# Optimization experiments

Hardware: AMD Instinct MI355X
Metric: run time of the kernel (lower is better)

Reference implementation:

```python
import jax, jax.numpy as jnp
import numpy as np
import math

B = 1048576
BG_RES = 512
NUM_LEVELS = 2
POWER = 4
MIPNOISE = 0.5
INIT_VAL = -2.0


def cube_face_uv(v):
    # v: [N,3] direction vectors. OpenGL cubemap face convention
    # (faces: 0:+x 1:-x 2:+y 3:-y 4:+z 5:-z), as used by nvdiffrast 'cube'.
    x, y, z = v[:, 0], v[:, 1], v[:, 2]
    ax, ay, az = jnp.abs(x), jnp.abs(y), jnp.abs(z)
    is_x = (ax >= ay) & (ax >= az)
    is_y = (~is_x) & (ay >= az)
    face = jnp.where(is_x, jnp.where(x >= 0, 0, 1),
                     jnp.where(is_y, jnp.where(y >= 0, 2, 3),
                               jnp.where(z >= 0, 4, 5))).astype(jnp.int32)
    ma = jnp.where(is_x, ax, jnp.where(is_y, ay, az))
    sc = jnp.where(is_x, jnp.where(x >= 0, -z, z),
                   jnp.where(is_y, x, jnp.where(z >= 0, x, -x)))
    tc = jnp.where(is_x, -y, jnp.where(is_y, jnp.where(y >= 0, z, -z), -y))
    u = 0.5 * (sc / ma + 1.0)
    t = 0.5 * (tc / ma + 1.0)
    return face, u, t


def build_pyramid(tex):
    # tex: [6,R,R,3] -> list of 2x2 box-filtered mips down to 1x1 (nvdiffrast style)
    levels = [tex]
    t = tex
    while t.shape[1] > 1:
        R = t.shape[1]
        t = t.reshape(6, R // 2, 2, R // 2, 2, 3).mean(axis=(2, 4))
        levels.append(t)
    return levels


def bilinear(tex, face, u, v):
    # tex: [6,R,R,3]; face/u/v: [N]. Clamp-to-edge bilinear per selected face.
    R = tex.shape[1]
    x = u * R - 0.5
    y = v * R - 0.5
    x0f = jnp.floor(x); y0f = jnp.floor(y)
    fx = (x - x0f)[:, None]; fy = (y - y0f)[:, None]
    x0 = jnp.clip(x0f.astype(jnp.int32), 0, R - 1)
    y0 = jnp.clip(y0f.astype(jnp.int32), 0, R - 1)
    x1 = jnp.clip(x0f.astype(jnp.int32) + 1, 0, R - 1)
    y1 = jnp.clip(y0f.astype(jnp.int32) + 1, 0, R - 1)
    flat = tex.reshape(6 * R * R, 3)
    base = face * (R * R)
    g00 = flat[base + y0 * R + x0]
    g01 = flat[base + y0 * R + x1]
    g10 = flat[base + y1 * R + x0]
    g11 = flat[base + y1 * R + x1]
    return ((1 - fx) * (1 - fy) * g00 + fx * (1 - fy) * g01 +
            (1 - fx) * fy * g10 + fx * fy * g11)


def sample_cubemap(tex6, face, u, v, mip):
    # trilinear: bilinear in two adjacent mips, lerp by fractional mip level
    levels = build_pyramid(tex6)
    lmax = float(len(levels) - 1)
    m = jnp.clip(mip, 0.0, lmax)
    out = jnp.zeros((face.shape[0], 3), tex6.dtype)
    for l, t in enumerate(levels):
        wl = jnp.clip(1.0 - jnp.abs(m - l), 0.0, 1.0)  # (1-f)/f trilinear weights
        out = out + wl[:, None] * bilinear(t, face, u, v)
    return out


def setup_inputs() -> dict:
    key = jax.random.key(0)
    k1, k2, k3, k4, k5 = jax.random.split(key, 5)
    viewdirs = jax.random.normal(k1, (B, 3), dtype=jnp.float32)
    viewdirs = viewdirs / jnp.linalg.norm(viewdirs, axis=-1, keepdims=True)
    saSample = jax.random.normal(k2, (B,), dtype=jnp.float32)
    noise_u = jax.random.uniform(k3, (B,), dtype=jnp.float32)
    # parameters (init_val*ones/(num_levels-i) in torch; perturbed for nontrivial grads)
    bg_mat0 = (INIT_VAL * jnp.ones((1, 6, 128, 128, 3), jnp.float32)
               + 0.1 * jax.random.normal(k4, (1, 6, 128, 128, 3), jnp.float32))
    bg_mat1 = (INIT_VAL / 2.0 * jnp.ones((1, 6, 512, 512, 3), jnp.float32)
               + 0.1 * jax.random.normal(k5, (1, 6, 512, 512, 3), jnp.float32))
    return {
        "viewdirs": viewdirs,
        "saSample": saSample,
        "noise_u": noise_u,
        "bg_mat0": bg_mat0,
        "bg_mat1": bg_mat1,
        "brightness": jnp.asarray(0.0, jnp.float32),
        "mul": jnp.asarray(1.0, jnp.float32),
        "mipbias": jnp.asarray(0.5, jnp.float32),
    }


def reference(viewdirs, saSample, noise_u, bg_mat0, bg_mat1, brightness, mul, mipbias):
    h = w = BG_RES  # from bg_mats[-1]
    # sa2mip
    distortion = 1.0 / jnp.max(jnp.abs(viewdirs), axis=-1)  # 1/||u||_inf
    saTexel = distortion / h / w
    miplevel = ((saSample - jnp.log(saTexel)) / math.log(POWER) / 2.0
                + mipbias + MIPNOISE * noise_u)
    miplevel = jnp.maximum(miplevel, 0.0)

    face, u, t = cube_face_uv(viewdirs)
    sumemb = sample_cubemap(bg_mat0[0], face, u, t, miplevel)  # mip 1 (128)
    sumemb = sumemb + sample_cubemap(bg_mat1[0], face, u, t, miplevel)  # mip 0 (512)

    # activation == 'identity' branch: exp(x).clip(0.01, 1000)
    img = jnp.clip(jnp.exp(jnp.clip(brightness, -1.0, 2.0) + mul * sumemb), 0.01, 1000.0)
    return img
```

## Files before the change

kernel.cpp:

```cpp
#include <hip/hip_runtime.h>
#include <math.h>


#define NPYR1_4 524286
#define FPB 557052
#define NFP 36780
#define NSTANDALONE 35988

__device__ __constant__ int OFFS0[7] = {0, 24576, 30720, 32256, 32640, 32736, 32760};
__device__ __constant__ int OFFS1[9] = {0, 393216, 491520, 516096, 522240,
                                        523776, 524160, 524256, 524280};
static const int H_OFFS0[5] = {0, 24576, 30720, 32256, 32640};
static const int H_OFFS1[5] = {0, 393216, 491520, 516096, 522240};

__device__ __constant__ int FPO1C[7] = {0, 25350, 31884, 33618, 34104, 34254, 34308};
__device__ __constant__ int FPO0C[5] = {34332, 36066, 36552, 36702, 36756};

__device__ __constant__ int FPB1T[4] = {33618, 34104, 34254, 34308};
__device__ __constant__ int FPB0T[2] = {36702, 36756};

__device__ __constant__ int S_START[7] = {0, 25350, 31884, 33618, 35352, 35838, 35988};
__device__ __constant__ int S_R[6]     = {64, 32, 16, 16, 8, 4};
__device__ __constant__ int S_SRC[6]   = {491520, 516096, 522240, 555006, 556542, 556926};
__device__ __constant__ int S_DST[6]   = {0, 25350, 31884, 34332, 36066, 36552};

struct PyrArgs {
    const float* src;
    float4* dst[5];
    int R;
    int tpf;
};

__global__ __launch_bounds__(256) void pyr_kernel(PyrArgs a0, PyrArgs a1, int split) {
    __shared__ float raw[32 * 96];
    __shared__ float4 A[16 * 16];
    __shared__ float4 Bb[8 * 8];

    PyrArgs a = (blockIdx.x < (unsigned)split) ? a0 : a1;
    int bid = (blockIdx.x < (unsigned)split) ? blockIdx.x : blockIdx.x - split;

    const int tpf = a.tpf, R = a.R;
    const int face = bid / (tpf * tpf);
    const int tif = bid - face * tpf * tpf;
    const int ty = tif / tpf, tx = tif - (tif / tpf) * tpf;
    const int tid = threadIdx.x;
    const int baseY = ty * 32, baseX = tx * 32;

    const float4* src4 = (const float4*)a.src;
    float4* raw4 = (float4*)raw;
    for (int idx = tid; idx < 768; idx += 256) {
        int r = idx / 24, c = idx - (idx / 24) * 24;
        size_t fidx = ((size_t)(face * R + baseY + r) * R + baseX) * 3;
        raw4[r * 24 + c] = src4[fidx / 4 + c];
    }
    __syncthreads();

    {
        int Rg = R >> 1;
        float4* dst = a.dst[0];
        int ly = tid >> 4, lx = tid & 15;
        const float* r0 = raw + (2 * ly) * 96 + 6 * lx;
        const float* r1 = r0 + 96;
        float4 s = make_float4(0.25f * (r0[0] + r0[3] + r1[0] + r1[3]),
                               0.25f * (r0[1] + r0[4] + r1[1] + r1[4]),
                               0.25f * (r0[2] + r0[5] + r1[2] + r1[5]), 0.f);
        A[tid] = s;
        dst[(size_t)(face * Rg + ty * 16 + ly) * Rg + tx * 16 + lx] = s;
    }
    __syncthreads();

    float4* cur = A;
    float4* nxt = Bb;
    int curT = 16;
    for (int l = 1; l < 5; ++l) {
        const int nT = curT >> 1;
        const int Rg = R >> (l + 1);
        const int tb = 32 >> (l + 1);
        float4* dst = a.dst[l];
        const int n = nT * nT;
        for (int idx = tid; idx < n; idx += 256) {
            int ly = idx / nT, lx = idx - (idx / nT) * nT;
            float4 q00 = cur[(2 * ly) * curT + 2 * lx];
            float4 q01 = cur[(2 * ly) * curT + 2 * lx + 1];
            float4 q10 = cur[(2 * ly + 1) * curT + 2 * lx];
            float4 q11 = cur[(2 * ly + 1) * curT + 2 * lx + 1];
            float4 s = make_float4(0.25f * (q00.x + q01.x + q10.x + q11.x),
                                   0.25f * (q00.y + q01.y + q10.y + q11.y),
                                   0.25f * (q00.z + q01.z + q10.z + q11.z), 0.f);
            nxt[ly * nT + lx] = s;
            dst[(size_t)(face * Rg + ty * tb + ly) * Rg + tx * tb + lx] = s;
        }
        __syncthreads();
        float4* tmp = cur; cur = nxt; nxt = tmp;
        curT = nT;
    }
}

__global__ __launch_bounds__(256) void tail_fp_kernel(const float4* __restrict__ ws4,
                                                      float4* __restrict__ fp4) {
    __shared__ float4 A[16 * 16];
    __shared__ float4 Bb[8 * 8];
    const int tid = threadIdx.x;
    const int b = blockIdx.x;

    if (b < 12) {
        const int isP0 = (b >= 6) ? 1 : 0;
        const int face = isP0 ? (b - 6) : b;
        const int R0 = isP0 ? 4 : 16;
        const int nlev = isP0 ? 2 : 4;
        const int srcoff = isP0 ? (NPYR1_4 + 32640) : 522240;
        const float4* src = ws4 + srcoff + (size_t)face * R0 * R0;
        for (int idx = tid; idx < R0 * R0; idx += 256) A[idx] = src[idx];
        __syncthreads();

        float4* cur = A;
        float4* nxt = Bb;
        int curT = R0;
        for (int l = 0; l < nlev; ++l) {
            const int nT = curT >> 1;
            for (int idx = tid; idx < nT * nT; idx += 256) {
                int ly = idx / nT, lx = idx - (idx / nT) * nT;
                float4 q00 = cur[(2 * ly) * curT + 2 * lx];
                float4 q01 = cur[(2 * ly) * curT + 2 * lx + 1];
                float4 q10 = cur[(2 * ly + 1) * curT + 2 * lx];
                float4 q11 = cur[(2 * ly + 1) * curT + 2 * lx + 1];
                nxt[ly * nT + lx] =
                    make_float4(0.25f * (q00.x + q01.x + q10.x + q11.x),
                                0.25f * (q00.y + q01.y + q10.y + q11.y),
                                0.25f * (q00.z + q01.z + q10.z + q11.z), 0.f);
            }
            __syncthreads();
            const int Rl = nT, per1 = Rl + 1;
            const int fpbase = (isP0 ? FPB0T[l] : FPB1T[l]) + face * per1 * per1;
            for (int idx = tid; idx < per1 * per1; idx += 256) {
                int j = idx / per1, i = idx - (idx / per1) * per1;
                int x0 = max(i - 1, 0), x1 = min(i, Rl - 1);
                int y0 = max(j - 1, 0), y1 = min(j, Rl - 1);
                float4 q00 = nxt[y0 * Rl + x0];
                float4 q01 = nxt[y0 * Rl + x1];
                float4 q10 = nxt[y1 * Rl + x0];
                float4 q11 = nxt[y1 * Rl + x1];
                size_t d = (size_t)(fpbase + idx) * 4;
                fp4[d]     = make_float4(q00.x, q00.y, q00.z, q01.x);
                fp4[d + 1] = make_float4(q01.y, q01.z, q10.x, q10.y);
                fp4[d + 2] = make_float4(q10.z, q11.x, q11.y, q11.z);
            }
            __syncthreads();
            float4* tmp = cur; cur = nxt; nxt = tmp;
            curT = nT;
        }
    } else {
        int t = (b - 12) * 256 + tid;
        if (t >= NSTANDALONE) return;
        int s = 0;
#pragma unroll
        for (int k = 1; k <= 5; ++k)
            if (t >= S_START[k]) s = k;
        int local = t - S_START[s];
        int R = S_R[s];
        int per1 = R + 1;
        int per = per1 * per1;
        int face = local / per;
        int rem = local - face * per;
        int j = rem / per1;
        int i = rem - j * per1;
        const float4* fb = ws4 + S_SRC[s] + (size_t)face * R * R;
        int x0 = max(i - 1, 0), x1 = min(i, R - 1);
        int y0 = max(j - 1, 0), y1 = min(j, R - 1);
        float4 q00 = fb[y0 * R + x0];
        float4 q01 = fb[y0 * R + x1];
        float4 q10 = fb[y1 * R + x0];
        float4 q11 = fb[y1 * R + x1];
        size_t d = (size_t)(S_DST[s] + local) * 4;
        fp4[d]     = make_float4(q00.x, q00.y, q00.z, q01.x);
        fp4[d + 1] = make_float4(q01.y, q01.z, q10.x, q10.y);
        fp4[d + 2] = make_float4(q10.z, q11.x, q11.y, q11.z);
    }
}

__device__ __forceinline__ void sample_level_fp(const float4* __restrict__ fp, int R,
                                                int face, float u, float v, float o[3]) {
    float xf = u * (float)R - 0.5f;
    float yf = v * (float)R - 0.5f;
    float x0f = floorf(xf), y0f = floorf(yf);
    float fx = xf - x0f, fy = yf - y0f;
    int i = min(max((int)x0f + 1, 0), R);
    int j = min(max((int)y0f + 1, 0), R);
    int per1 = R + 1;
    size_t base = (size_t)((face * per1 + j) * per1 + i) * 4;
    float4 A  = fp[base];
    float4 Bq = fp[base + 1];
    float4 C  = fp[base + 2];
    float w00 = (1.f - fx) * (1.f - fy);
    float w01 = fx * (1.f - fy);
    float w10 = (1.f - fx) * fy;
    float w11 = fx * fy;
    o[0] = w00 * A.x + w01 * A.w + w10 * Bq.z + w11 * C.y;
    o[1] = w00 * A.y + w01 * Bq.x + w10 * Bq.w + w11 * C.z;
    o[2] = w00 * A.z + w01 * Bq.y + w10 * C.x + w11 * C.w;
}

__device__ __forceinline__ void bilin4(const float4* __restrict__ tex, int R,
                                       int face, float u, float v, float o[3]) {
    float xf = u * (float)R - 0.5f;
    float yf = v * (float)R - 0.5f;
    float x0f = floorf(xf), y0f = floorf(yf);
    float fx = xf - x0f, fy = yf - y0f;
    int xi = (int)x0f, yi = (int)y0f;
    int x0 = min(max(xi, 0), R - 1);
    int x1 = min(max(xi + 1, 0), R - 1);
    int y0 = min(max(yi, 0), R - 1);
    int y1 = min(max(yi + 1, 0), R - 1);
    const float4* base = tex + (size_t)face * R * R;
    float4 p00 = base[y0 * R + x0];
    float4 p01 = base[y0 * R + x1];
    float4 p10 = base[y1 * R + x0];
    float4 p11 = base[y1 * R + x1];
    float w00 = (1.f - fx) * (1.f - fy);
    float w01 = fx * (1.f - fy);
    float w10 = (1.f - fx) * fy;
    float w11 = fx * fy;
    o[0] = w00 * p00.x + w01 * p01.x + w10 * p10.x + w11 * p11.x;
    o[1] = w00 * p00.y + w01 * p01.y + w10 * p10.y + w11 * p11.y;
    o[2] = w00 * p00.z + w01 * p01.z + w10 * p10.z + w11 * p11.z;
}

__device__ __forceinline__ void bilin3(const float* __restrict__ tex, int R,
                                       int face, float u, float v, float o[3]) {
    float xf = u * (float)R - 0.5f;
    float yf = v * (float)R - 0.5f;
    float x0f = floorf(xf), y0f = floorf(yf);
    float fx = xf - x0f, fy = yf - y0f;
    int xi = (int)x0f, yi = (int)y0f;
    int x0 = min(max(xi, 0), R - 1);
    int x1 = min(max(xi + 1, 0), R - 1);
    int y0 = min(max(yi, 0), R - 1);
    int y1 = min(max(yi + 1, 0), R - 1);
    const float* base = tex + (size_t)face * R * R * 3;
    const float* p00 = base + (y0 * R + x0) * 3;
    const float* p01 = base + (y0 * R + x1) * 3;
    const float* p10 = base + (y1 * R + x0) * 3;
    const float* p11 = base + (y1 * R + x1) * 3;
    float w00 = (1.f - fx) * (1.f - fy);
    float w01 = fx * (1.f - fy);
    float w10 = (1.f - fx) * fy;
    float w11 = fx * fy;
#pragma unroll
    for (int c = 0; c < 3; ++c)
        o[c] = w00 * p00[c] + w01 * p01[c] + w10 * p10[c] + w11 * p11[c];
}

__device__ __forceinline__ void sample_pyr(const float* __restrict__ base_tex,
                                           const float4* __restrict__ pyr,
                                           const int* offs,
                                           const float4* __restrict__ fp4,
                                           const int* fpoffs,
                                           int lmax, int R0,
                                           int face, float u, float v, float mip,
                                           float o[3]) {
    float m = fminf(fmaxf(mip, 0.f), (float)lmax);
    float l0f = floorf(m);
    int l0 = (int)l0f;
    float f = m - l0f;
    float c0[3];
    if (l0 >= 3)
        sample_level_fp(fp4 + (size_t)fpoffs[l0 - 3] * 4, R0 >> l0, face, u, v, c0);
    else if (l0 == 0)
        bilin3(base_tex, R0, face, u, v, c0);
    else
        bilin4(pyr + offs[l0 - 1], R0 >> l0, face, u, v, c0);
    if (f > 0.f && l0 < lmax) {
        float c1[3];
        int l1 = l0 + 1;
        if (l1 >= 3)
            sample_level_fp(fp4 + (size_t)fpoffs[l1 - 3] * 4, R0 >> l1, face, u, v, c1);
        else
            bilin4(pyr + offs[l1 - 1], R0 >> l1, face, u, v, c1);
        float w0 = 1.f - f;
#pragma unroll
        for (int c = 0; c < 3; ++c) o[c] = w0 * c0[c] + f * c1[c];
    } else {
#pragma unroll
        for (int c = 0; c < 3; ++c) o[c] = c0[c];
    }
}

__global__ __launch_bounds__(256) void sample_kernel(
    const float* __restrict__ vd, const float* __restrict__ sa,
    const float* __restrict__ nu, const float* __restrict__ tex0,
    const float* __restrict__ tex1, const float* __restrict__ sb,
    const float* __restrict__ sm, const float* __restrict__ smb,
    const float4* __restrict__ pyr0, const float4* __restrict__ pyr1,
    const float4* __restrict__ fp4, float* __restrict__ out, int n) {
    int i = blockIdx.x * 256 + threadIdx.x;
    if (i >= n) return;

    float x = vd[3 * i + 0];
    float y = vd[3 * i + 1];
    float z = vd[3 * i + 2];
    float ax = fabsf(x), ay = fabsf(y), az = fabsf(z);

    bool is_x = (ax >= ay) && (ax >= az);
    bool is_y = (!is_x) && (ay >= az);

    int face;
    float ma, sc, tc;
    if (is_x) {
        face = (x >= 0.f) ? 0 : 1;
        ma = ax;
        sc = (x >= 0.f) ? -z : z;
        tc = -y;
    } else if (is_y) {
        face = (y >= 0.f) ? 2 : 3;
        ma = ay;
        sc = x;
        tc = (y >= 0.f) ? z : -z;
    } else {
        face = (z >= 0.f) ? 4 : 5;
        ma = az;
        sc = (z >= 0.f) ? x : -x;
        tc = -y;
    }
    float rma = __frcp_rn(ma);
    float u = 0.5f * (sc * rma + 1.f);
    float t = 0.5f * (tc * rma + 1.f);

    float mip = (sa[i] + 12.476649250079015f + __logf(ma)) * 0.36067376022224085f +
                smb[0] + 0.5f * nu[i];
    mip = fmaxf(mip, 0.f);

    float l0f = floorf(mip);
    int l0 = (int)l0f;
    float f = mip - l0f;

    float s0[3], s1[3];
    bool fast = (l0 >= 3) && (l0 < 7);
    if (__all(fast)) {
        int oA = (l0 == 3) ? 0     : (l0 == 4) ? 25350 : (l0 == 5) ? 31884 : 33618;
        int oB = (l0 == 3) ? 25350 : (l0 == 4) ? 31884 : (l0 == 5) ? 33618 : 34104;
        int oC = (l0 == 3) ? 34332 : (l0 == 4) ? 36066 : (l0 == 5) ? 36552 : 36702;
        int oD = (l0 == 3) ? 36066 : (l0 == 4) ? 36552 : (l0 == 5) ? 36702 : 36756;
        float a0v[3], a1v[3], b0v[3], b1v[3];
        sample_level_fp(fp4 + (size_t)oA * 4, 512 >> l0, face, u, t, a0v);
        sample_level_fp(fp4 + (size_t)oB * 4, 512 >> (l0 + 1), face, u, t, a1v);
        sample_level_fp(fp4 + (size_t)oC * 4, 128 >> l0, face, u, t, b0v);
        sample_level_fp(fp4 + (size_t)oD * 4, 128 >> (l0 + 1), face, u, t, b1v);
        float w0 = 1.f - f;
#pragma unroll
        for (int c = 0; c < 3; ++c) {
            s0[c] = w0 * a1v[c] * 0.f + (w0 * a0v[c] + f * a1v[c]);
            s0[c] = w0 * a0v[c] + f * a1v[c];
            s1[c] = w0 * b0v[c] + f * b1v[c];
        }
    } else {
        sample_pyr(tex0, pyr0, OFFS0, fp4, FPO0C, 7, 128, face, u, t, mip, s0);
        sample_pyr(tex1, pyr1, OFFS1, fp4, FPO1C, 9, 512, face, u, t, mip, s1);
    }

    float b = fminf(fmaxf(sb[0], -1.f), 2.f);
    float mul = sm[0];
#pragma unroll
    for (int c = 0; c < 3; ++c) {
        float e = __expf(b + mul * (s0[c] + s1[c]));
        out[3 * i + c] = fminf(fmaxf(e, 0.01f), 1000.f);
    }
}

extern "C" void kernel_launch(void* const* d_in, const int* in_sizes, int n_in,
                              void* d_out, int out_size, void* d_ws, size_t ws_size,
                              hipStream_t stream) {
    const float* vd = (const float*)d_in[0];
    const float* sa = (const float*)d_in[1];
    const float* nu = (const float*)d_in[2];
    const float* tex0 = (const float*)d_in[3];
    const float* tex1 = (const float*)d_in[4];
    const float* br = (const float*)d_in[5];
    const float* mu = (const float*)d_in[6];
    const float* mb = (const float*)d_in[7];
    float* out = (float*)d_out;

    float4* pyr1 = (float4*)d_ws;
    float4* pyr0 = pyr1 + NPYR1_4;
    float4* fp4 = pyr1 + FPB;

    const int B = in_sizes[1];

    PyrArgs a0{}, a1{};
    a0.src = tex1; a0.R = 512; a0.tpf = 16;
    for (int l = 0; l < 5; ++l) a0.dst[l] = pyr1 + H_OFFS1[l];
    a1.src = tex0; a1.R = 128; a1.tpf = 4;
    for (int l = 0; l < 5; ++l) a1.dst[l] = pyr0 + H_OFFS0[l];
    int split1 = 6 * 16 * 16;
    int grid1 = split1 + 6 * 4 * 4;
    hipLaunchKernelGGL(pyr_kernel, dim3(grid1), dim3(256), 0, stream, a0, a1, split1);

    int grid2 = 12 + (NSTANDALONE + 255) / 256;
    hipLaunchKernelGGL(tail_fp_kernel, dim3(grid2), dim3(256), 0, stream,
                       (const float4*)d_ws, fp4);

    int grid = (B + 255) / 256;
    hipLaunchKernelGGL(sample_kernel, dim3(grid), dim3(256), 0, stream,
                       vd, sa, nu, tex0, tex1, br, mu, mb, pyr0, pyr1, fp4, out, B);
}
```

Baseline: 119.4 us.

## Fuse pyramid, footprint and sampling into one cooperative persistent kernel

```diff
diff --git a/kernel.cpp b/kernel.cpp
--- a/kernel.cpp
+++ b/kernel.cpp
@@ -1,17 +1,20 @@
 #include <hip/hip_runtime.h>
+#include <hip/hip_cooperative_groups.h>
 #include <math.h>
+
+namespace cg = cooperative_groups;
 
 
 #define NPYR1_4 524286
 #define FPB 557052
 #define NFP 36780
 #define NSTANDALONE 35988
+#define NT1 1536
+#define NTILES 1632
 
 __device__ __constant__ int OFFS0[7] = {0, 24576, 30720, 32256, 32640, 32736, 32760};
 __device__ __constant__ int OFFS1[9] = {0, 393216, 491520, 516096, 522240,
                                         523776, 524160, 524256, 524280};
-static const int H_OFFS0[5] = {0, 24576, 30720, 32256, 32640};
-static const int H_OFFS1[5] = {0, 393216, 491520, 516096, 522240};
 
 __device__ __constant__ int FPO1C[7] = {0, 25350, 31884, 33618, 34104, 34254, 34308};
 __device__ __constant__ int FPO0C[5] = {34332, 36066, 36552, 36702, 36756};
@@ -24,29 +27,17 @@
 __device__ __constant__ int S_SRC[6]   = {491520, 516096, 522240, 555006, 556542, 556926};
 __device__ __constant__ int S_DST[6]   = {0, 25350, 31884, 34332, 36066, 36552};
 
-struct PyrArgs {
-    const float* src;
-    float4* dst[5];
-    int R;
-    int tpf;
-};
-
-__global__ __launch_bounds__(256) void pyr_kernel(PyrArgs a0, PyrArgs a1, int split) {
-    __shared__ float raw[32 * 96];
-    __shared__ float4 A[16 * 16];
-    __shared__ float4 Bb[8 * 8];
-
-    PyrArgs a = (blockIdx.x < (unsigned)split) ? a0 : a1;
-    int bid = (blockIdx.x < (unsigned)split) ? blockIdx.x : blockIdx.x - split;
-
-    const int tpf = a.tpf, R = a.R;
-    const int face = bid / (tpf * tpf);
-    const int tif = bid - face * tpf * tpf;
+
+__device__ __forceinline__ void pyr_tile(const float* __restrict__ src, int R, int tpf,
+                                         int tix, float4* __restrict__ pbase,
+                                         const int* offs, int tid,
+                                         float* raw, float4* A, float4* Bb) {
+    const int face = tix / (tpf * tpf);
+    const int tif = tix - face * tpf * tpf;
     const int ty = tif / tpf, tx = tif - (tif / tpf) * tpf;
-    const int tid = threadIdx.x;
     const int baseY = ty * 32, baseX = tx * 32;
 
-    const float4* src4 = (const float4*)a.src;
+    const float4* src4 = (const float4*)src;
     float4* raw4 = (float4*)raw;
     for (int idx = tid; idx < 768; idx += 256) {
         int r = idx / 24, c = idx - (idx / 24) * 24;
@@ -57,7 +48,7 @@
 
     {
         int Rg = R >> 1;
-        float4* dst = a.dst[0];
+        float4* dst = pbase + offs[0];
         int ly = tid >> 4, lx = tid & 15;
         const float* r0 = raw + (2 * ly) * 96 + 6 * lx;
         const float* r1 = r0 + 96;
@@ -76,7 +67,7 @@
         const int nT = curT >> 1;
         const int Rg = R >> (l + 1);
         const int tb = 32 >> (l + 1);
-        float4* dst = a.dst[l];
+        float4* dst = pbase + offs[l];
         const int n = nT * nT;
         for (int idx = tid; idx < n; idx += 256) {
             int ly = idx / nT, lx = idx - (idx / nT) * nT;
@@ -96,13 +87,9 @@
     }
 }
 
-__global__ __launch_bounds__(256) void tail_fp_kernel(const float4* __restrict__ ws4,
-                                                      float4* __restrict__ fp4) {
-    __shared__ float4 A[16 * 16];
-    __shared__ float4 Bb[8 * 8];
-    const int tid = threadIdx.x;
-    const int b = blockIdx.x;
-
+__device__ __forceinline__ void tail_fp_body(const float4* __restrict__ ws4,
+                                             float4* __restrict__ fp4,
+                                             int b, int tid, float4* A, float4* Bb) {
     if (b < 12) {
         const int isP0 = (b >= 6) ? 1 : 0;
         const int face = isP0 ? (b - 6) : b;
@@ -151,30 +138,31 @@
         }
     } else {
         int t = (b - 12) * 256 + tid;
-        if (t >= NSTANDALONE) return;
-        int s = 0;
-#pragma unroll
-        for (int k = 1; k <= 5; ++k)
-            if (t >= S_START[k]) s = k;
-        int local = t - S_START[s];
-        int R = S_R[s];
-        int per1 = R + 1;
-        int per = per1 * per1;
-        int face = local / per;
-        int rem = local - face * per;
-        int j = rem / per1;
-        int i = rem - j * per1;
-        const float4* fb = ws4 + S_SRC[s] + (size_t)face * R * R;
-        int x0 = max(i - 1, 0), x1 = min(i, R - 1);
-        int y0 = max(j - 1, 0), y1 = min(j, R - 1);
-        float4 q00 = fb[y0 * R + x0];
-        float4 q01 = fb[y0 * R + x1];
-        float4 q10 = fb[y1 * R + x0];
-        float4 q11 = fb[y1 * R + x1];
-        size_t d = (size_t)(S_DST[s] + local) * 4;
-        fp4[d]     = make_float4(q00.x, q00.y, q00.z, q01.x);
-        fp4[d + 1] = make_float4(q01.y, q01.z, q10.x, q10.y);
-        fp4[d + 2] = make_float4(q10.z, q11.x, q11.y, q11.z);
+        if (t < NSTANDALONE) {
+            int s = 0;
+#pragma unroll
+            for (int k = 1; k <= 5; ++k)
+                if (t >= S_START[k]) s = k;
+            int local = t - S_START[s];
+            int R = S_R[s];
+            int per1 = R + 1;
+            int per = per1 * per1;
+            int face = local / per;
+            int rem = local - face * per;
+            int j = rem / per1;
+            int i = rem - j * per1;
+            const float4* fb = ws4 + S_SRC[s] + (size_t)face * R * R;
+            int x0 = max(i - 1, 0), x1 = min(i, R - 1);
+            int y0 = max(j - 1, 0), y1 = min(j, R - 1);
+            float4 q00 = fb[y0 * R + x0];
+            float4 q01 = fb[y0 * R + x1];
+            float4 q10 = fb[y1 * R + x0];
+            float4 q11 = fb[y1 * R + x1];
+            size_t d = (size_t)(S_DST[s] + local) * 4;
+            fp4[d]     = make_float4(q00.x, q00.y, q00.z, q01.x);
+            fp4[d + 1] = make_float4(q01.y, q01.z, q10.x, q10.y);
+            fp4[d + 2] = make_float4(q10.z, q11.x, q11.y, q11.z);
+        }
     }
 }
 
@@ -285,16 +273,12 @@
     }
 }
 
-__global__ __launch_bounds__(256) void sample_kernel(
-    const float* __restrict__ vd, const float* __restrict__ sa,
+__device__ __forceinline__ void sample_ray(
+    int i, const float* __restrict__ vd, const float* __restrict__ sa,
     const float* __restrict__ nu, const float* __restrict__ tex0,
-    const float* __restrict__ tex1, const float* __restrict__ sb,
-    const float* __restrict__ sm, const float* __restrict__ smb,
+    const float* __restrict__ tex1, float sbc, float mulc, float smbc,
     const float4* __restrict__ pyr0, const float4* __restrict__ pyr1,
-    const float4* __restrict__ fp4, float* __restrict__ out, int n) {
-    int i = blockIdx.x * 256 + threadIdx.x;
-    if (i >= n) return;
-
+    const float4* __restrict__ fp4, float* __restrict__ out) {
     float x = vd[3 * i + 0];
     float y = vd[3 * i + 1];
     float z = vd[3 * i + 2];
@@ -326,7 +310,7 @@
     float t = 0.5f * (tc * rma + 1.f);
 
     float mip = (sa[i] + 12.476649250079015f + __logf(ma)) * 0.36067376022224085f +
-                smb[0] + 0.5f * nu[i];
+                smbc + 0.5f * nu[i];
     mip = fmaxf(mip, 0.f);
 
     float l0f = floorf(mip);
@@ -348,7 +332,6 @@
         float w0 = 1.f - f;
 #pragma unroll
         for (int c = 0; c < 3; ++c) {
-            s0[c] = w0 * a1v[c] * 0.f + (w0 * a0v[c] + f * a1v[c]);
             s0[c] = w0 * a0v[c] + f * a1v[c];
             s1[c] = w0 * b0v[c] + f * b1v[c];
         }
@@ -357,14 +340,92 @@
         sample_pyr(tex1, pyr1, OFFS1, fp4, FPO1C, 9, 512, face, u, t, mip, s1);
     }
 
-    float b = fminf(fmaxf(sb[0], -1.f), 2.f);
-    float mul = sm[0];
 #pragma unroll
     for (int c = 0; c < 3; ++c) {
-        float e = __expf(b + mul * (s0[c] + s1[c]));
+        float e = __expf(sbc + mulc * (s0[c] + s1[c]));
         out[3 * i + c] = fminf(fmaxf(e, 0.01f), 1000.f);
     }
 }
+
+
+struct KArgs {
+    const float* vd; const float* sa; const float* nu;
+    const float* tex0; const float* tex1;
+    const float* sb; const float* sm; const float* smb;
+    float4* ws4;
+    float4* fp4;
+    float* out;
+    int n;
+};
+
+__global__ __launch_bounds__(256, 4) void mega_kernel(KArgs a) {
+    __shared__ float raw[32 * 96];
+    __shared__ float4 A[16 * 16];
+    __shared__ float4 Bb[8 * 8];
+
+    cg::grid_group grid = cg::this_grid();
+    const int tid = threadIdx.x;
+    const int b = blockIdx.x;
+    float4* pyr1 = a.ws4;
+    float4* pyr0 = a.ws4 + NPYR1_4;
+
+    for (int t = b; t < NTILES; t += gridDim.x) {
+        if (t < NT1)
+            pyr_tile(a.tex1, 512, 16, t, pyr1, OFFS1, tid, raw, A, Bb);
+        else
+            pyr_tile(a.tex0, 128, 4, t - NT1, pyr0, OFFS0, tid, raw, A, Bb);
+    }
+    grid.sync();
+
+    if (b < 12 + (NSTANDALONE + 255) / 256)
+        tail_fp_body(a.ws4, a.fp4, b, tid, A, Bb);
+    grid.sync();
+
+    {
+        float sbc = fminf(fmaxf(a.sb[0], -1.f), 2.f);
+        float mulc = a.sm[0];
+        float smbc = a.smb[0];
+        const int stride = gridDim.x << 8;
+        for (int i = (b << 8) + tid; i < a.n; i += stride)
+            sample_ray(i, a.vd, a.sa, a.nu, a.tex0, a.tex1, sbc, mulc, smbc,
+                       pyr0, pyr1, a.fp4, a.out);
+    }
+}
+
+
+__global__ __launch_bounds__(256) void pyr_kernel_fb(const float* __restrict__ t1,
+                                                     const float* __restrict__ t0,
+                                                     float4* pyr1, float4* pyr0) {
+    __shared__ float raw[32 * 96];
+    __shared__ float4 A[16 * 16];
+    __shared__ float4 Bb[8 * 8];
+    int b = blockIdx.x;
+    if (b < NT1)
+        pyr_tile(t1, 512, 16, b, pyr1, OFFS1, threadIdx.x, raw, A, Bb);
+    else
+        pyr_tile(t0, 128, 4, b - NT1, pyr0, OFFS0, threadIdx.x, raw, A, Bb);
+}
+
+__global__ __launch_bounds__(256) void tail_fp_kernel_fb(const float4* __restrict__ ws4,
+                                                         float4* __restrict__ fp4) {
+    __shared__ float4 A[16 * 16];
+    __shared__ float4 Bb[8 * 8];
+    tail_fp_body(ws4, fp4, blockIdx.x, threadIdx.x, A, Bb);
+}
+
+__global__ __launch_bounds__(256) void sample_kernel_fb(
+    const float* __restrict__ vd, const float* __restrict__ sa,
+    const float* __restrict__ nu, const float* __restrict__ tex0,
+    const float* __restrict__ tex1, const float* __restrict__ sb,
+    const float* __restrict__ sm, const float* __restrict__ smb,
+    const float4* __restrict__ pyr0, const float4* __restrict__ pyr1,
+    const float4* __restrict__ fp4, float* __restrict__ out, int n) {
+    int i = blockIdx.x * 256 + threadIdx.x;
+    if (i >= n) return;
+    float sbc = fminf(fmaxf(sb[0], -1.f), 2.f);
+    sample_ray(i, vd, sa, nu, tex0, tex1, sbc, sm[0], smb[0], pyr0, pyr1, fp4, out);
+}
+
 
 extern "C" void kernel_launch(void* const* d_in, const int* in_sizes, int n_in,
                               void* d_out, int out_size, void* d_ws, size_t ws_size,
@@ -385,20 +446,40 @@
 
     const int B = in_sizes[1];
 
-    PyrArgs a0{}, a1{};
-    a0.src = tex1; a0.R = 512; a0.tpf = 16;
-    for (int l = 0; l < 5; ++l) a0.dst[l] = pyr1 + H_OFFS1[l];
-    a1.src = tex0; a1.R = 128; a1.tpf = 4;
-    for (int l = 0; l < 5; ++l) a1.dst[l] = pyr0 + H_OFFS0[l];
-    int split1 = 6 * 16 * 16;
-    int grid1 = split1 + 6 * 4 * 4;
-    hipLaunchKernelGGL(pyr_kernel, dim3(grid1), dim3(256), 0, stream, a0, a1, split1);
-
-    int grid2 = 12 + (NSTANDALONE + 255) / 256;
-    hipLaunchKernelGGL(tail_fp_kernel, dim3(grid2), dim3(256), 0, stream,
-                       (const float4*)d_ws, fp4);
-
-    int grid = (B + 255) / 256;
-    hipLaunchKernelGGL(sample_kernel, dim3(grid), dim3(256), 0, stream,
-                       vd, sa, nu, tex0, tex1, br, mu, mb, pyr0, pyr1, fp4, out, B);
-}
+    static int coopBlocks = -2;
+    if (coopBlocks == -2) {
+        int nb = 0;
+        hipError_t e = hipOccupancyMaxActiveBlocksPerMultiprocessor(&nb, mega_kernel, 256, 0);
+        if (e != hipSuccess || nb <= 0) {
+            coopBlocks = -1;
+        } else {
+            int g = nb * 256;
+            if (g > 2048) g = 2048;
+            coopBlocks = (g >= 256) ? g : -1;
+        }
+    }
+
+    bool launched = false;
+    if (coopBlocks > 0) {
+        KArgs ka;
+        ka.vd = vd; ka.sa = sa; ka.nu = nu; ka.tex0 = tex0; ka.tex1 = tex1;
+        ka.sb = br; ka.sm = mu; ka.smb = mb;
+        ka.ws4 = pyr1; ka.fp4 = fp4; ka.out = out; ka.n = B;
+        void* kargs[] = {(void*)&ka};
+        hipError_t e = hipLaunchCooperativeKernel(mega_kernel, dim3(coopBlocks),
+                                                  dim3(256), kargs, 0, stream);
+        if (e == hipSuccess) launched = true;
+        else coopBlocks = -1;
+    }
+
+    if (!launched) {
+        hipLaunchKernelGGL(pyr_kernel_fb, dim3(NTILES), dim3(256), 0, stream,
+                           tex1, tex0, pyr1, pyr0);
+        int grid2 = 12 + (NSTANDALONE + 255) / 256;
+        hipLaunchKernelGGL(tail_fp_kernel_fb, dim3(grid2), dim3(256), 0, stream,
+                           (const float4*)d_ws, fp4);
+        int grid = (B + 255) / 256;
+        hipLaunchKernelGGL(sample_kernel_fb, dim3(grid), dim3(256), 0, stream,
+                           vd, sa, nu, tex0, tex1, br, mu, mb, pyr0, pyr1, fp4, out, B);
+    }
+}
```

New measurement: 256.2 us. 2.15x slower.
